# Optimization experiments

Measured on AMD Instinct MI355X. Metric: run time of the kernel, lower is better.

## Reference

```python
import jax, jax.numpy as jnp
import numpy as np

D_MODEL = 384
D_INNER = 768   # 2 * d_model
D_STATE = 16
DT_RANK = 24    # ceil(d_model/16)
K_CONV = 4
BATCH = 8
SEQ = 2048
EPS = 1e-5


def _layer_norm(x, w, b):
    mu = x.mean(-1, keepdims=True)
    var = ((x - mu) ** 2).mean(-1, keepdims=True)
    return (x - mu) * jax.lax.rsqrt(var + EPS) * w + b


def _silu(x):
    return x * jax.nn.sigmoid(x)


def _mamba_mixer(x, in_proj, conv_w, conv_b, x_proj, dt_w, dt_b, A_log, Dp, out_proj):
    # x: (B, L, d_model)
    xz = x @ in_proj.T                      # (B, L, 2*d_inner)
    xs, z = jnp.split(xz, 2, axis=-1)       # each (B, L, d_inner)
    # causal depthwise conv1d (pad left k-1)
    xc = jnp.transpose(xs, (0, 2, 1))       # (B, d_inner, L)
    xc = jnp.pad(xc, ((0, 0), (0, 0), (K_CONV - 1, 0)))
    xc = jax.lax.conv_general_dilated(
        xc, conv_w, window_strides=(1,), padding='VALID',
        feature_group_count=D_INNER,
        dimension_numbers=('NCH', 'OIH', 'NCH'))
    xs = _silu(jnp.transpose(xc, (0, 2, 1)) + conv_b)   # (B, L, d_inner)
    # input-dependent SSM parameters
    x_dbl = xs @ x_proj.T                    # (B, L, dt_rank + 2*d_state)
    dt, Bm, Cm = jnp.split(x_dbl, [DT_RANK, DT_RANK + D_STATE], axis=-1)
    dt = jax.nn.softplus(dt @ dt_w.T + dt_b)  # (B, L, d_inner)
    A = -jnp.exp(A_log)                       # (d_inner, d_state)

    def step(h, inp):
        dt_t, B_t, C_t, x_t = inp             # (B,d), (B,N), (B,N), (B,d)
        h = jnp.exp(dt_t[:, :, None] * A) * h + (dt_t * x_t)[:, :, None] * B_t[:, None, :]
        y = jnp.einsum('bdn,bn->bd', h, C_t)
        return h, y

    h0 = jnp.zeros((xs.shape[0], D_INNER, D_STATE), xs.dtype)
    inps = (jnp.moveaxis(dt, 1, 0), jnp.moveaxis(Bm, 1, 0),
            jnp.moveaxis(Cm, 1, 0), jnp.moveaxis(xs, 1, 0))
    _, ys = jax.lax.scan(step, h0, inps)      # ys: (L, B, d_inner)
    y = jnp.moveaxis(ys, 0, 1) + xs * Dp      # skip term D*x
    y = y * _silu(z)                          # gated output
    return y @ out_proj.T                     # (B, L, d_model)


def setup_inputs() -> dict:
    key = jax.random.key(0)
    ks = jax.random.split(key, 10)
    s = 0.02
    A_init = jnp.broadcast_to(jnp.log(jnp.arange(1, D_STATE + 1, dtype=jnp.float32)),
                              (2, D_INNER, D_STATE))
    return {
        'x': jax.random.normal(ks[0], (BATCH, SEQ, D_MODEL), jnp.float32),
        'norm_w': jnp.ones((2, D_MODEL), jnp.float32),
        'norm_b': jnp.zeros((2, D_MODEL), jnp.float32),
        'in_proj': jax.random.normal(ks[1], (2, 2 * D_INNER, D_MODEL)) * s,
        'conv_w': jax.random.normal(ks[2], (2, D_INNER, 1, K_CONV)) * 0.2,
        'conv_b': jax.random.normal(ks[3], (2, D_INNER)) * s,
        'x_proj': jax.random.normal(ks[4], (2, DT_RANK + 2 * D_STATE, D_INNER)) * s,
        'dt_w': jax.random.normal(ks[5], (2, D_INNER, DT_RANK)) * s,
        'dt_b': jax.random.normal(ks[6], (2, D_INNER)) * 0.1 - 4.0,
        'A_log': A_init,
        'Dp': jnp.ones((2, D_INNER), jnp.float32),
        'out_proj': jax.random.normal(ks[7], (2, D_MODEL, D_INNER)) * s,
    }


def reference(x, norm_w, norm_b, in_proj, conv_w, conv_b, x_proj, dt_w, dt_b, A_log, Dp, out_proj):
    def blk(i, h):
        return h + _mamba_mixer(_layer_norm(h, norm_w[i], norm_b[i]),
                                in_proj[i], conv_w[i], conv_b[i], x_proj[i],
                                dt_w[i], dt_b[i], A_log[i], Dp[i], out_proj[i])
    h = blk(0, x)                    # forward-direction block
    h = jnp.flip(h, axis=-2)         # reverse sequence
    h = blk(1, h)                    # backward-direction block
    return jnp.flip(h, axis=-2)      # restore order
```

## Files before the change

kernel.cpp:

```cpp
#include <hip/hip_runtime.h>
#include <hip/hip_bf16.h>
#include <cstddef>

#define D_MODEL 384
#define D_INNER 768
#define D_STATE 16
#define DT_RANK 24
#define K_CONV  4
#define BATCH   8
#define SEQ     2048
#define BL      (BATCH * SEQ)
#define NCHUNK  128
#define LCHUNK  (SEQ / NCHUNK)
#define XDBL_LD 64
#define LOG2E   1.44269504088896f

typedef unsigned short ushort_t;
typedef __bf16 bf16x8 __attribute__((ext_vector_type(8)));
typedef float  f32x4  __attribute__((ext_vector_type(4)));
typedef unsigned short u16x8 __attribute__((ext_vector_type(8)));

#define GLOBAL_AS(p) ((const __attribute__((address_space(1))) void*)(p))
#define LDS_AS(p)    ((__attribute__((address_space(3))) void*)(p))

__device__ __forceinline__ ushort_t f32_to_bf16_rne(float v) {
    unsigned int u = __float_as_uint(v);
    return (ushort_t)((u + 0x7FFFu + ((u >> 16) & 1u)) >> 16);
}
__device__ __forceinline__ float bf16_to_f32(ushort_t u) {
    return __uint_as_float(((unsigned int)u) << 16);
}

__device__ __forceinline__ void pow_tree16(float w1, float* pw) {
    float w2 = w1 * w1, w4 = w2 * w2, w8 = w4 * w4;
    pw[0] = w1;        pw[1] = w2;        pw[2] = w2 * w1;   pw[3] = w4;
    pw[4] = w4 * w1;   pw[5] = w4 * w2;   pw[6] = w4 * pw[2]; pw[7] = w8;
    pw[8] = w8 * w1;   pw[9] = w8 * w2;   pw[10] = w8 * pw[2]; pw[11] = w8 * w4;
    pw[12] = w8 * pw[4]; pw[13] = w8 * pw[5]; pw[14] = w8 * pw[6]; pw[15] = w8 * w8;
}

__global__ __launch_bounds__(256) void cast_bf16_kernel(
    const float* __restrict__ in, ushort_t* __restrict__ out, int n)
{
    int i = blockIdx.x * 256 + threadIdx.x;
    if (i < n) out[i] = f32_to_bf16_rne(in[i]);
}

__global__ __launch_bounds__(256) void cast_xproj_kernel(
    const float* __restrict__ in, ushort_t* __restrict__ out)
{
    int i = blockIdx.x * 256 + threadIdx.x;
    if (i >= 2 * 64 * D_INNER) return;
    int c   = i % D_INNER;
    int r   = (i / D_INNER) % 64;
    int dir = i / (64 * D_INNER);
    out[i] = (r < 56) ? f32_to_bf16_rne(in[((size_t)dir * 56 + r) * D_INNER + c])
                      : (ushort_t)0;
}

__global__ __launch_bounds__(256) void prep_transpose_kernel(
    const float* __restrict__ conv_w, const float* __restrict__ A_log,
    const float* __restrict__ dt_w, float* __restrict__ cwt,
    float* __restrict__ alt, float* __restrict__ dwt)
{
    int i = blockIdx.x * 256 + threadIdx.x;
    const int NCW = 2 * K_CONV * D_INNER;
    const int NAL = 2 * D_STATE * D_INNER;
    const int NDW = 2 * DT_RANK * D_INNER;
    if (i < NCW) {
        int c = i % D_INNER, k = (i / D_INNER) % K_CONV, dir = i / (K_CONV * D_INNER);
        cwt[i] = conv_w[((size_t)dir * D_INNER + c) * K_CONV + k];
    } else if (i < NCW + NAL) {
        int j = i - NCW;
        int d = j % D_INNER, n = (j / D_INNER) % D_STATE, dir = j / (D_STATE * D_INNER);
        alt[j] = A_log[((size_t)dir * D_INNER + d) * D_STATE + n];
    } else if (i < NCW + NAL + NDW) {
        int j = i - NCW - NAL;
        int d = j % D_INNER, r = (j / D_INNER) % DT_RANK, dir = j / (DT_RANK * D_INNER);
        dwt[j] = dt_w[((size_t)dir * D_INNER + d) * DT_RANK + r];
    }
}

__global__ __launch_bounds__(256) void check_A_kernel(
    const float* __restrict__ A_log, int* __restrict__ flags)
{
    __shared__ int ok[2];
    int tid = threadIdx.x;
    if (tid < 2) ok[tid] = 1;
    __syncthreads();
    for (int dir = 0; dir < 2; dir++) {
        bool good = true;
        for (int j = tid; j < D_INNER * D_STATE; j += 256) {
            int n = j % D_STATE;
            float v = __expf(A_log[(size_t)dir * D_INNER * D_STATE + j]);
            good = good && (fabsf(v - (float)(n + 1)) <= 1e-4f * (float)(n + 1));
        }
        if (!good) atomicAnd(&ok[dir], 0);
    }
    __syncthreads();
    if (tid < 2) flags[tid] = ok[tid];
}

__global__ __launch_bounds__(384) void ln_kernel(
    const float* __restrict__ in, const float* __restrict__ w,
    const float* __restrict__ b, ushort_t* __restrict__ out)
{
    int row = blockIdx.x;
    int tid = threadIdx.x;
    float v = in[(size_t)row * D_MODEL + tid];
    float s = v, sq = v * v;
    #pragma unroll
    for (int o = 32; o; o >>= 1) {
        s  += __shfl_down(s, o);
        sq += __shfl_down(sq, o);
    }
    __shared__ float ss[6], ssq[6];
    __shared__ float mb[2];
    int wid = tid >> 6;
    if ((tid & 63) == 0) { ss[wid] = s; ssq[wid] = sq; }
    __syncthreads();
    if (tid == 0) {
        float S = 0.f, Q = 0.f;
        #pragma unroll
        for (int k = 0; k < 6; k++) { S += ss[k]; Q += ssq[k]; }
        float mu  = S * (1.0f / D_MODEL);
        float var = Q * (1.0f / D_MODEL) - mu * mu;
        mb[0] = mu;
        mb[1] = rsqrtf(var + 1e-5f);
    }
    __syncthreads();
    float r = (v - mb[0]) * mb[1] * w[tid] + b[tid];
    out[(size_t)row * D_MODEL + tid] = f32_to_bf16_rne(r);
}

__global__ __launch_bounds__(256) void gemm_mfma_b16(
    const ushort_t* __restrict__ A, const ushort_t* __restrict__ W,
    ushort_t* __restrict__ C, int N, int K)
{
    __shared__ __bf16 As[128 * 32];
    __shared__ __bf16 Ws[128 * 32];
    int tid  = threadIdx.x;
    int bm = blockIdx.x, bn = blockIdx.y;
    int lane = tid & 63, wave = tid >> 6;
    int wr = wave >> 1, wc = wave & 1;
    int quad = lane >> 4, l16 = lane & 15;

    const ushort_t* Ag = A + (size_t)(bm * 128 + (tid >> 2)) * K + (tid & 3) * 8;
    const ushort_t* Wg = W + (size_t)(bn * 128 + (tid >> 2)) * K + (tid & 3) * 8;

    f32x4 acc[4][4] = {};

    for (int k0 = 0; k0 < K; k0 += 32) {
        __syncthreads();
        __builtin_amdgcn_global_load_lds(GLOBAL_AS(Ag + k0),
                                         LDS_AS(As + tid * 8), 16, 0, 0);
        __builtin_amdgcn_global_load_lds(GLOBAL_AS(Ag + (size_t)64 * K + k0),
                                         LDS_AS(As + 2048 + tid * 8), 16, 0, 0);
        __builtin_amdgcn_global_load_lds(GLOBAL_AS(Wg + k0),
                                         LDS_AS(Ws + tid * 8), 16, 0, 0);
        __builtin_amdgcn_global_load_lds(GLOBAL_AS(Wg + (size_t)64 * K + k0),
                                         LDS_AS(Ws + 2048 + tid * 8), 16, 0, 0);
        __syncthreads();

        bf16x8 af[4], wf[4];
        #pragma unroll
        for (int i = 0; i < 4; i++)
            af[i] = *(const bf16x8*)(As + (wr * 64 + i * 16 + l16) * 32 + quad * 8);
        #pragma unroll
        for (int j = 0; j < 4; j++)
            wf[j] = *(const bf16x8*)(Ws + (wc * 64 + j * 16 + l16) * 32 + quad * 8);
        #pragma unroll
        for (int i = 0; i < 4; i++)
            #pragma unroll
            for (int j = 0; j < 4; j++)
                acc[i][j] = __builtin_amdgcn_mfma_f32_16x16x32_bf16(
                    af[i], wf[j], acc[i][j], 0, 0, 0);
    }

    #pragma unroll
    for (int i = 0; i < 4; i++) {
        #pragma unroll
        for (int r = 0; r < 4; r++) {
            int row = bm * 128 + wr * 64 + i * 16 + quad * 4 + r;
            #pragma unroll
            for (int j = 0; j < 4; j++) {
                int col = bn * 128 + wc * 64 + j * 16 + l16;
                C[(size_t)row * N + col] = f32_to_bf16_rne(acc[i][j][r]);
            }
        }
    }
}

__global__ __launch_bounds__(256) void gemm_mfma_f32(
    const ushort_t* __restrict__ A, const ushort_t* __restrict__ W,
    const float* __restrict__ resid, float* __restrict__ C, int N, int K)
{
    __shared__ __bf16 As[128 * 32];
    __shared__ __bf16 Ws[128 * 32];
    int tid  = threadIdx.x;
    int bm = blockIdx.x, bn = blockIdx.y;
    int lane = tid & 63, wave = tid >> 6;
    int wr = wave >> 1, wc = wave & 1;
    int quad = lane >> 4, l16 = lane & 15;

    const ushort_t* Ag = A + (size_t)(bm * 128 + (tid >> 2)) * K + (tid & 3) * 8;
    const ushort_t* Wg = W + (size_t)(bn * 128 + (tid >> 2)) * K + (tid & 3) * 8;

    f32x4 acc[4][4] = {};

    for (int k0 = 0; k0 < K; k0 += 32) {
        __syncthreads();
        __builtin_amdgcn_global_load_lds(GLOBAL_AS(Ag + k0),
                                         LDS_AS(As + tid * 8), 16, 0, 0);
        __builtin_amdgcn_global_load_lds(GLOBAL_AS(Ag + (size_t)64 * K + k0),
                                         LDS_AS(As + 2048 + tid * 8), 16, 0, 0);
        __builtin_amdgcn_global_load_lds(GLOBAL_AS(Wg + k0),
                                         LDS_AS(Ws + tid * 8), 16, 0, 0);
        __builtin_amdgcn_global_load_lds(GLOBAL_AS(Wg + (size_t)64 * K + k0),
                                         LDS_AS(Ws + 2048 + tid * 8), 16, 0, 0);
        __syncthreads();

        bf16x8 af[4], wf[4];
        #pragma unroll
        for (int i = 0; i < 4; i++)
            af[i] = *(const bf16x8*)(As + (wr * 64 + i * 16 + l16) * 32 + quad * 8);
        #pragma unroll
        for (int j = 0; j < 4; j++)
            wf[j] = *(const bf16x8*)(Ws + (wc * 64 + j * 16 + l16) * 32 + quad * 8);
        #pragma unroll
        for (int i = 0; i < 4; i++)
            #pragma unroll
            for (int j = 0; j < 4; j++)
                acc[i][j] = __builtin_amdgcn_mfma_f32_16x16x32_bf16(
                    af[i], wf[j], acc[i][j], 0, 0, 0);
    }

    #pragma unroll
    for (int i = 0; i < 4; i++) {
        #pragma unroll
        for (int r = 0; r < 4; r++) {
            int row = bm * 128 + wr * 64 + i * 16 + quad * 4 + r;
            #pragma unroll
            for (int j = 0; j < 4; j++) {
                int col = bn * 128 + wc * 64 + j * 16 + l16;
                size_t idx = (size_t)row * N + col;
                C[idx] = acc[i][j][r] + resid[idx];
            }
        }
    }
}

__global__ __launch_bounds__(256) void xdbl_mfma(
    const ushort_t* __restrict__ A, const ushort_t* __restrict__ W,
    float* __restrict__ C)
{
    __shared__ __bf16 As[128 * 32];
    __shared__ __bf16 Ws[64 * 32];
    int tid  = threadIdx.x;
    int bm = blockIdx.x;
    int lane = tid & 63, wave = tid >> 6;
    int quad = lane >> 4, l16 = lane & 15;

    const ushort_t* Ag = A + (size_t)(bm * 128 + (tid >> 2)) * D_INNER + (tid & 3) * 8;
    const ushort_t* Wg = W + (size_t)(tid >> 2) * D_INNER + (tid & 3) * 8;

    f32x4 acc[2][4] = {};

    for (int k0 = 0; k0 < D_INNER; k0 += 32) {
        __syncthreads();
        __builtin_amdgcn_global_load_lds(GLOBAL_AS(Ag + k0),
                                         LDS_AS(As + tid * 8), 16, 0, 0);
        __builtin_amdgcn_global_load_lds(GLOBAL_AS(Ag + (size_t)64 * D_INNER + k0),
                                         LDS_AS(As + 2048 + tid * 8), 16, 0, 0);
        __builtin_amdgcn_global_load_lds(GLOBAL_AS(Wg + k0),
                                         LDS_AS(Ws + tid * 8), 16, 0, 0);
        __syncthreads();

        bf16x8 af[2], wf[4];
        #pragma unroll
        for (int i = 0; i < 2; i++)
            af[i] = *(const bf16x8*)(As + (wave * 32 + i * 16 + l16) * 32 + quad * 8);
        #pragma unroll
        for (int j = 0; j < 4; j++)
            wf[j] = *(const bf16x8*)(Ws + (j * 16 + l16) * 32 + quad * 8);
        #pragma unroll
        for (int i = 0; i < 2; i++)
            #pragma unroll
            for (int j = 0; j < 4; j++)
                acc[i][j] = __builtin_amdgcn_mfma_f32_16x16x32_bf16(
                    af[i], wf[j], acc[i][j], 0, 0, 0);
    }

    #pragma unroll
    for (int i = 0; i < 2; i++) {
        #pragma unroll
        for (int r = 0; r < 4; r++) {
            int row = bm * 128 + wave * 32 + i * 16 + quad * 4 + r;
            #pragma unroll
            for (int j = 0; j < 4; j++) {
                int col = j * 16 + l16;
                C[(size_t)row * XDBL_LD + col] = acc[i][j][r];
            }
        }
    }
}

__global__ __launch_bounds__(256) void dt_kernel(
    const float* __restrict__ xdbl, const float* __restrict__ dwt,
    const float* __restrict__ dtbias, ushort_t* __restrict__ dtb)
{
    int g    = blockIdx.x % 3;
    int row0 = (blockIdx.x / 3) * 16;
    int tid  = threadIdx.x;
    int d    = g * 256 + tid;
    float w[DT_RANK];
    #pragma unroll
    for (int r = 0; r < DT_RANK; r++) w[r] = dwt[r * D_INNER + d];
    float bias = dtbias[d];
    __shared__ float xd[16][DT_RANK];
    if (tid < 16 * DT_RANK) {
        int rr = tid / DT_RANK, cc = tid % DT_RANK;
        xd[rr][cc] = xdbl[(size_t)(row0 + rr) * XDBL_LD + cc];
    }
    __syncthreads();
    #pragma unroll 4
    for (int i = 0; i < 16; i++) {
        float acc = bias;
        #pragma unroll
        for (int r = 0; r < DT_RANK; r++) acc = fmaf(xd[i][r], w[r], acc);
        float sp = acc > 20.f ? acc : __logf(1.f + __expf(acc));
        dtb[(size_t)(row0 + i) * D_INNER + d] = f32_to_bf16_rne(sp);
    }
}

__global__ __launch_bounds__(256) void conv_silu_kernel(
    const ushort_t* __restrict__ xz, const float* __restrict__ cwt,
    const float* __restrict__ cb, ushort_t* __restrict__ xsc, int dir)
{
    int idx8 = blockIdx.x * 256 + threadIdx.x;
    int c8   = (idx8 % 96) * 8;
    int row  = idx8 / 96;
    int l    = row % SEQ;
    int b0   = row - l;

    float acc[8];
    float4 bv0 = *(const float4*)(cb + c8);
    float4 bv1 = *(const float4*)(cb + c8 + 4);
    acc[0] = bv0.x; acc[1] = bv0.y; acc[2] = bv0.z; acc[3] = bv0.w;
    acc[4] = bv1.x; acc[5] = bv1.y; acc[6] = bv1.z; acc[7] = bv1.w;

    #pragma unroll
    for (int k = 0; k < 4; k++) {
        int ls = dir ? (l + k) : (l - 3 + k);
        int wk = dir ? (3 - k) : k;
        bool ok = dir ? (ls < SEQ) : (ls >= 0);
        if (ok) {
            u16x8 v = *(const u16x8*)(xz + (size_t)(b0 + ls) * 1536 + c8);
            float4 w0 = *(const float4*)(cwt + wk * D_INNER + c8);
            float4 w1 = *(const float4*)(cwt + wk * D_INNER + c8 + 4);
            float wv[8] = {w0.x, w0.y, w0.z, w0.w, w1.x, w1.y, w1.z, w1.w};
            #pragma unroll
            for (int j = 0; j < 8; j++)
                acc[j] = fmaf(bf16_to_f32(v[j]), wv[j], acc[j]);
        }
    }
    u16x8 o;
    #pragma unroll
    for (int j = 0; j < 8; j++) {
        float sg = 1.0f / (1.0f + __expf(-acc[j]));
        o[j] = f32_to_bf16_rne(acc[j] * sg);
    }
    *(u16x8*)(xsc + (size_t)row * D_INNER + c8) = o;
}

__global__ __launch_bounds__(256) void scan_pass1(
    const ushort_t* __restrict__ xsc, const ushort_t* __restrict__ dtb,
    const float* __restrict__ xdbl, const float* __restrict__ alt,
    const int* __restrict__ flag,
    ushort_t* __restrict__ hstate, float* __restrict__ sumdt_buf, int dir)
{
    int g = blockIdx.x % 3;
    int c = (blockIdx.x / 3) % NCHUNK;
    int b = blockIdx.x / (3 * NCHUNK);
    int d = g * 256 + threadIdx.x;
    float h[D_STATE] = {};
    float sdt = 0.f;
    size_t base = (size_t)b * SEQ;

    if (flag[0]) {
        for (int i = 0; i < LCHUNK; i++) {
            int p = c * LCHUNK + i;
            int l = dir ? (SEQ - 1 - p) : p;
            size_t row = base + l;
            float dtv = bf16_to_f32(dtb[row * D_INNER + d]);
            float xv  = bf16_to_f32(xsc[row * D_INNER + d]);
            float dtx = dtv * xv;
            sdt += dtv;
            const float* Br = xdbl + row * XDBL_LD + DT_RANK;
            float pw[D_STATE];
            pow_tree16(__builtin_amdgcn_exp2f(-dtv * LOG2E), pw);
            #pragma unroll
            for (int n = 0; n < D_STATE; n++)
                h[n] = fmaf(pw[n], h[n], dtx * Br[n]);
        }
    } else {
        float A2[D_STATE];
        #pragma unroll
        for (int n = 0; n < D_STATE; n++)
            A2[n] = -__expf(alt[n * D_INNER + d]) * LOG2E;
        for (int i = 0; i < LCHUNK; i++) {
            int p = c * LCHUNK + i;
            int l = dir ? (SEQ - 1 - p) : p;
            size_t row = base + l;
            float dtv = bf16_to_f32(dtb[row * D_INNER + d]);
            float xv  = bf16_to_f32(xsc[row * D_INNER + d]);
            float dtx = dtv * xv;
            sdt += dtv;
            const float* Br = xdbl + row * XDBL_LD + DT_RANK;
            #pragma unroll
            for (int n = 0; n < D_STATE; n++)
                h[n] = fmaf(__builtin_amdgcn_exp2f(dtv * A2[n]), h[n], dtx * Br[n]);
        }
    }
    size_t cidx = (size_t)(b * NCHUNK + c) * D_INNER + d;
    sumdt_buf[cidx] = sdt;
    #pragma unroll
    for (int n = 0; n < D_STATE; n++)
        hstate[cidx * D_STATE + n] = f32_to_bf16_rne(h[n]);
}

__global__ __launch_bounds__(256) void scan_pass2(
    ushort_t* __restrict__ hstate, const float* __restrict__ sumdt_buf,
    const float* __restrict__ alt)
{
    int gid = blockIdx.x * 256 + threadIdx.x;
    int n = gid & 15;
    int d = (gid >> 4) % D_INNER;
    int b = gid / (16 * D_INNER);
    float A2 = -__expf(alt[n * D_INNER + d]) * LOG2E;
    float h = 0.f;
    for (int c = 0; c < NCHUNK; c++) {
        size_t cidx = (size_t)(b * NCHUNK + c) * D_INNER + d;
        float ho = bf16_to_f32(hstate[cidx * D_STATE + n]);
        hstate[cidx * D_STATE + n] = f32_to_bf16_rne(h);
        h = fmaf(__builtin_amdgcn_exp2f(A2 * sumdt_buf[cidx]), h, ho);
    }
}

__global__ __launch_bounds__(256) void scan_pass3(
    const ushort_t* __restrict__ xsc, const ushort_t* __restrict__ dtb,
    const ushort_t* __restrict__ xz, const float* __restrict__ xdbl,
    const float* __restrict__ alt, const float* __restrict__ Dp,
    const int* __restrict__ flag, const ushort_t* __restrict__ hstate,
    ushort_t* __restrict__ y, int dir)
{
    int g = blockIdx.x % 3;
    int c = (blockIdx.x / 3) % NCHUNK;
    int b = blockIdx.x / (3 * NCHUNK);
    int d = g * 256 + threadIdx.x;
    size_t cidx = (size_t)(b * NCHUNK + c) * D_INNER + d;
    float h[D_STATE];
    #pragma unroll
    for (int n = 0; n < D_STATE; n++)
        h[n] = bf16_to_f32(hstate[cidx * D_STATE + n]);
    float Dd = Dp[d];
    size_t base = (size_t)b * SEQ;

    if (flag[0]) {
        for (int i = 0; i < LCHUNK; i++) {
            int p = c * LCHUNK + i;
            int l = dir ? (SEQ - 1 - p) : p;
            size_t row = base + l;
            float dtv = bf16_to_f32(dtb[row * D_INNER + d]);
            float xv  = bf16_to_f32(xsc[row * D_INNER + d]);
            float zv  = bf16_to_f32(xz[row * 1536 + D_INNER + d]);
            float dtx = dtv * xv;
            const float* Br = xdbl + row * XDBL_LD + DT_RANK;
            const float* Cr = Br + D_STATE;
            float pw[D_STATE];
            pow_tree16(__builtin_amdgcn_exp2f(-dtv * LOG2E), pw);
            float yv = 0.f;
            #pragma unroll
            for (int n = 0; n < D_STATE; n++) {
                h[n] = fmaf(pw[n], h[n], dtx * Br[n]);
                yv = fmaf(h[n], Cr[n], yv);
            }
            yv = fmaf(xv, Dd, yv);
            float sg = 1.f / (1.f + __expf(-zv));
            yv *= zv * sg;
            y[row * D_INNER + d] = f32_to_bf16_rne(yv);
        }
    } else {
        float A2[D_STATE];
        #pragma unroll
        for (int n = 0; n < D_STATE; n++)
            A2[n] = -__expf(alt[n * D_INNER + d]) * LOG2E;
        for (int i = 0; i < LCHUNK; i++) {
            int p = c * LCHUNK + i;
            int l = dir ? (SEQ - 1 - p) : p;
            size_t row = base + l;
            float dtv = bf16_to_f32(dtb[row * D_INNER + d]);
            float xv  = bf16_to_f32(xsc[row * D_INNER + d]);
            float zv  = bf16_to_f32(xz[row * 1536 + D_INNER + d]);
            float dtx = dtv * xv;
            const float* Br = xdbl + row * XDBL_LD + DT_RANK;
            const float* Cr = Br + D_STATE;
            float yv = 0.f;
            #pragma unroll
            for (int n = 0; n < D_STATE; n++) {
                h[n] = fmaf(__builtin_amdgcn_exp2f(dtv * A2[n]), h[n], dtx * Br[n]);
                yv = fmaf(h[n], Cr[n], yv);
            }
            yv = fmaf(xv, Dd, yv);
            float sg = 1.f / (1.f + __expf(-zv));
            yv *= zv * sg;
            y[row * D_INNER + d] = f32_to_bf16_rne(yv);
        }
    }
}

extern "C" void kernel_launch(void* const* d_in, const int* in_sizes, int n_in,
                              void* d_out, int out_size, void* d_ws, size_t ws_size,
                              hipStream_t stream)
{
    const float* x       = (const float*)d_in[0];
    const float* norm_w  = (const float*)d_in[1];
    const float* norm_b  = (const float*)d_in[2];
    const float* in_proj = (const float*)d_in[3];
    const float* conv_w  = (const float*)d_in[4];
    const float* conv_b  = (const float*)d_in[5];
    const float* x_proj  = (const float*)d_in[6];
    const float* dt_w    = (const float*)d_in[7];
    const float* dt_b    = (const float*)d_in[8];
    const float* A_log   = (const float*)d_in[9];
    const float* Dp      = (const float*)d_in[10];
    const float* out_proj= (const float*)d_in[11];
    float* out = (float*)d_out;

    float* ws   = (float*)d_ws;
    float* reg0 = ws;                ws += (size_t)BL * D_INNER / 2;
    ushort_t* lnb = (ushort_t*)reg0;
    ushort_t* ybf = (ushort_t*)reg0;
    ushort_t* xzb  = (ushort_t*)ws;  ws += (size_t)BL * 1536 / 2;
    ushort_t* xscb = (ushort_t*)ws;  ws += (size_t)BL * D_INNER / 2;
    ushort_t* dtb  = (ushort_t*)ws;  ws += (size_t)BL * D_INNER / 2;
    float* xdbl = ws;                ws += (size_t)BL * XDBL_LD;
    float* sumdt  = ws;              ws += (size_t)BATCH * NCHUNK * D_INNER;
    ushort_t* hstate = (ushort_t*)ws; ws += (size_t)BATCH * NCHUNK * D_INNER * D_STATE / 2;
    ushort_t* wbf_in  = (ushort_t*)ws;  ws += (size_t)2 * 1536 * D_MODEL / 2;
    ushort_t* wbf_out = (ushort_t*)ws;  ws += (size_t)2 * D_MODEL * D_INNER / 2;
    ushort_t* xp_bf   = (ushort_t*)ws;  ws += (size_t)2 * 64 * D_INNER / 2;
    float* cwt = ws;                 ws += (size_t)2 * K_CONV * D_INNER;
    float* alt = ws;                 ws += (size_t)2 * D_STATE * D_INNER;
    float* dwt = ws;                 ws += (size_t)2 * DT_RANK * D_INNER;
    int* aflags = (int*)ws;          ws += 2;

    cast_bf16_kernel<<<(2 * 1536 * D_MODEL + 255) / 256, 256, 0, stream>>>(
        in_proj, wbf_in, 2 * 1536 * D_MODEL);
    cast_bf16_kernel<<<(2 * D_MODEL * D_INNER + 255) / 256, 256, 0, stream>>>(
        out_proj, wbf_out, 2 * D_MODEL * D_INNER);
    cast_xproj_kernel<<<(2 * 64 * D_INNER + 255) / 256, 256, 0, stream>>>(
        x_proj, xp_bf);
    {
        int total = 2 * (K_CONV + D_STATE + DT_RANK) * D_INNER;
        prep_transpose_kernel<<<(total + 255) / 256, 256, 0, stream>>>(
            conv_w, A_log, dt_w, cwt, alt, dwt);
    }
    check_A_kernel<<<1, 256, 0, stream>>>(A_log, aflags);

    for (int i = 0; i < 2; i++) {
        const float* hinp = (i == 0) ? x : out;
        ln_kernel<<<BL, 384, 0, stream>>>(hinp, norm_w + i * D_MODEL,
                                          norm_b + i * D_MODEL, lnb);
        gemm_mfma_b16<<<dim3(BL / 128, 1536 / 128), 256, 0, stream>>>(
            lnb, wbf_in + (size_t)i * 1536 * D_MODEL, xzb, 1536, D_MODEL);
        conv_silu_kernel<<<(BL * 96) / 256, 256, 0, stream>>>(
            xzb, cwt + (size_t)i * K_CONV * D_INNER, conv_b + i * D_INNER,
            xscb, i);
        xdbl_mfma<<<BL / 128, 256, 0, stream>>>(
            xscb, xp_bf + (size_t)i * 64 * D_INNER, xdbl);
        dt_kernel<<<(BL / 16) * 3, 256, 0, stream>>>(
            xdbl, dwt + (size_t)i * DT_RANK * D_INNER, dt_b + i * D_INNER, dtb);
        scan_pass1<<<BATCH * NCHUNK * 3, 256, 0, stream>>>(
            xscb, dtb, xdbl, alt + (size_t)i * D_STATE * D_INNER,
            aflags + i, hstate, sumdt, i);
        scan_pass2<<<(BATCH * D_INNER * D_STATE) / 256, 256, 0, stream>>>(
            hstate, sumdt, alt + (size_t)i * D_STATE * D_INNER);
        scan_pass3<<<BATCH * NCHUNK * 3, 256, 0, stream>>>(
            xscb, dtb, xzb, xdbl, alt + (size_t)i * D_STATE * D_INNER,
            Dp + i * D_INNER, aflags + i, hstate, ybf, i);
        gemm_mfma_f32<<<dim3(BL / 128, D_MODEL / 128), 256, 0, stream>>>(
            ybf, wbf_out + (size_t)i * D_MODEL * D_INNER, hinp, out,
            D_MODEL, D_INNER);
    }
}
```

Measured before the change: 499.8 us.

## Halve scan chunk count, widen GEMM K-tile to 64, merge prep kernels

Three separate changes. The chunked scan now uses 64 chunks instead of 128, so each chunk is longer and fewer chunk states are stored and combined. Both MFMA GEMMs now stage a 64-wide K slab per iteration instead of 32, which halves the barrier count and doubles LDS use. The four weight cast and transpose kernels are merged into one launch to cut launch overhead. The trade-offs are less scan parallelism per pass and lower occupancy from the larger LDS footprint.

```diff
diff --git a/kernel.cpp b/kernel.cpp
--- a/kernel.cpp
+++ b/kernel.cpp
@@ -10,7 +10,7 @@
 #define BATCH   8
 #define SEQ     2048
 #define BL      (BATCH * SEQ)
-#define NCHUNK  128
+#define NCHUNK  64
 #define LCHUNK  (SEQ / NCHUNK)
 #define XDBL_LD 64
 #define LOG2E   1.44269504088896f
@@ -39,45 +39,58 @@
     pw[12] = w8 * pw[4]; pw[13] = w8 * pw[5]; pw[14] = w8 * pw[6]; pw[15] = w8 * w8;
 }
 
-__global__ __launch_bounds__(256) void cast_bf16_kernel(
-    const float* __restrict__ in, ushort_t* __restrict__ out, int n)
+#define N_INP  (2 * 1536 * D_MODEL)
+#define N_OUTP (2 * D_MODEL * D_INNER)
+#define N_XP   (2 * 64 * D_INNER)
+#define N_CW   (2 * K_CONV * D_INNER)
+#define N_AL   (2 * D_STATE * D_INNER)
+#define N_DW   (2 * DT_RANK * D_INNER)
+#define N_PREP (N_INP + N_OUTP + N_XP + N_CW + N_AL + N_DW)
+
+__global__ __launch_bounds__(256) void prep_kernel(
+    const float* __restrict__ in_proj, const float* __restrict__ out_proj,
+    const float* __restrict__ x_proj, const float* __restrict__ conv_w,
+    const float* __restrict__ A_log, const float* __restrict__ dt_w,
+    ushort_t* __restrict__ wbf_in, ushort_t* __restrict__ wbf_out,
+    ushort_t* __restrict__ xp_bf, float* __restrict__ cwt,
+    float* __restrict__ alt, float* __restrict__ dwt)
 {
     int i = blockIdx.x * 256 + threadIdx.x;
-    if (i < n) out[i] = f32_to_bf16_rne(in[i]);
-}
-
-__global__ __launch_bounds__(256) void cast_xproj_kernel(
-    const float* __restrict__ in, ushort_t* __restrict__ out)
-{
-    int i = blockIdx.x * 256 + threadIdx.x;
-    if (i >= 2 * 64 * D_INNER) return;
-    int c   = i % D_INNER;
-    int r   = (i / D_INNER) % 64;
-    int dir = i / (64 * D_INNER);
-    out[i] = (r < 56) ? f32_to_bf16_rne(in[((size_t)dir * 56 + r) * D_INNER + c])
-                      : (ushort_t)0;
-}
-
-__global__ __launch_bounds__(256) void prep_transpose_kernel(
-    const float* __restrict__ conv_w, const float* __restrict__ A_log,
-    const float* __restrict__ dt_w, float* __restrict__ cwt,
-    float* __restrict__ alt, float* __restrict__ dwt)
-{
-    int i = blockIdx.x * 256 + threadIdx.x;
-    const int NCW = 2 * K_CONV * D_INNER;
-    const int NAL = 2 * D_STATE * D_INNER;
-    const int NDW = 2 * DT_RANK * D_INNER;
-    if (i < NCW) {
+    if (i < N_INP) {
+        wbf_in[i] = f32_to_bf16_rne(in_proj[i]);
+        return;
+    }
+    i -= N_INP;
+    if (i < N_OUTP) {
+        wbf_out[i] = f32_to_bf16_rne(out_proj[i]);
+        return;
+    }
+    i -= N_OUTP;
+    if (i < N_XP) {
+        int c   = i % D_INNER;
+        int r   = (i / D_INNER) % 64;
+        int dir = i / (64 * D_INNER);
+        xp_bf[i] = (r < 56)
+            ? f32_to_bf16_rne(x_proj[((size_t)dir * 56 + r) * D_INNER + c])
+            : (ushort_t)0;
+        return;
+    }
+    i -= N_XP;
+    if (i < N_CW) {
         int c = i % D_INNER, k = (i / D_INNER) % K_CONV, dir = i / (K_CONV * D_INNER);
         cwt[i] = conv_w[((size_t)dir * D_INNER + c) * K_CONV + k];
-    } else if (i < NCW + NAL) {
-        int j = i - NCW;
-        int d = j % D_INNER, n = (j / D_INNER) % D_STATE, dir = j / (D_STATE * D_INNER);
-        alt[j] = A_log[((size_t)dir * D_INNER + d) * D_STATE + n];
-    } else if (i < NCW + NAL + NDW) {
-        int j = i - NCW - NAL;
-        int d = j % D_INNER, r = (j / D_INNER) % DT_RANK, dir = j / (DT_RANK * D_INNER);
-        dwt[j] = dt_w[((size_t)dir * D_INNER + d) * DT_RANK + r];
+        return;
+    }
+    i -= N_CW;
+    if (i < N_AL) {
+        int d = i % D_INNER, n = (i / D_INNER) % D_STATE, dir = i / (D_STATE * D_INNER);
+        alt[i] = A_log[((size_t)dir * D_INNER + d) * D_STATE + n];
+        return;
+    }
+    i -= N_AL;
+    if (i < N_DW) {
+        int d = i % D_INNER, r = (i / D_INNER) % DT_RANK, dir = i / (DT_RANK * D_INNER);
+        dwt[i] = dt_w[((size_t)dir * D_INNER + d) * DT_RANK + r];
     }
 }
 
@@ -137,44 +150,48 @@
     const ushort_t* __restrict__ A, const ushort_t* __restrict__ W,
     ushort_t* __restrict__ C, int N, int K)
 {
-    __shared__ __bf16 As[128 * 32];
-    __shared__ __bf16 Ws[128 * 32];
+    __shared__ __bf16 As[128 * 64];
+    __shared__ __bf16 Ws[128 * 64];
     int tid  = threadIdx.x;
     int bm = blockIdx.x, bn = blockIdx.y;
     int lane = tid & 63, wave = tid >> 6;
     int wr = wave >> 1, wc = wave & 1;
     int quad = lane >> 4, l16 = lane & 15;
 
-    const ushort_t* Ag = A + (size_t)(bm * 128 + (tid >> 2)) * K + (tid & 3) * 8;
-    const ushort_t* Wg = W + (size_t)(bn * 128 + (tid >> 2)) * K + (tid & 3) * 8;
+    const ushort_t* Ag = A + (size_t)(bm * 128 + (tid >> 3)) * K + (tid & 7) * 8;
+    const ushort_t* Wg = W + (size_t)(bn * 128 + (tid >> 3)) * K + (tid & 7) * 8;
 
     f32x4 acc[4][4] = {};
 
-    for (int k0 = 0; k0 < K; k0 += 32) {
+    for (int k0 = 0; k0 < K; k0 += 64) {
         __syncthreads();
-        __builtin_amdgcn_global_load_lds(GLOBAL_AS(Ag + k0),
-                                         LDS_AS(As + tid * 8), 16, 0, 0);
-        __builtin_amdgcn_global_load_lds(GLOBAL_AS(Ag + (size_t)64 * K + k0),
-                                         LDS_AS(As + 2048 + tid * 8), 16, 0, 0);
-        __builtin_amdgcn_global_load_lds(GLOBAL_AS(Wg + k0),
-                                         LDS_AS(Ws + tid * 8), 16, 0, 0);
-        __builtin_amdgcn_global_load_lds(GLOBAL_AS(Wg + (size_t)64 * K + k0),
-                                         LDS_AS(Ws + 2048 + tid * 8), 16, 0, 0);
+        #pragma unroll
+        for (int s = 0; s < 4; s++) {
+            __builtin_amdgcn_global_load_lds(
+                GLOBAL_AS(Ag + (size_t)(s * 32) * K + k0),
+                LDS_AS(As + s * 2048 + tid * 8), 16, 0, 0);
+            __builtin_amdgcn_global_load_lds(
+                GLOBAL_AS(Wg + (size_t)(s * 32) * K + k0),
+                LDS_AS(Ws + s * 2048 + tid * 8), 16, 0, 0);
+        }
         __syncthreads();
 
-        bf16x8 af[4], wf[4];
-        #pragma unroll
-        for (int i = 0; i < 4; i++)
-            af[i] = *(const bf16x8*)(As + (wr * 64 + i * 16 + l16) * 32 + quad * 8);
-        #pragma unroll
-        for (int j = 0; j < 4; j++)
-            wf[j] = *(const bf16x8*)(Ws + (wc * 64 + j * 16 + l16) * 32 + quad * 8);
-        #pragma unroll
-        for (int i = 0; i < 4; i++)
+        #pragma unroll
+        for (int ks = 0; ks < 64; ks += 32) {
+            bf16x8 af[4], wf[4];
+            #pragma unroll
+            for (int i = 0; i < 4; i++)
+                af[i] = *(const bf16x8*)(As + (wr * 64 + i * 16 + l16) * 64 + ks + quad * 8);
             #pragma unroll
             for (int j = 0; j < 4; j++)
-                acc[i][j] = __builtin_amdgcn_mfma_f32_16x16x32_bf16(
-                    af[i], wf[j], acc[i][j], 0, 0, 0);
+                wf[j] = *(const bf16x8*)(Ws + (wc * 64 + j * 16 + l16) * 64 + ks + quad * 8);
+            #pragma unroll
+            for (int i = 0; i < 4; i++)
+                #pragma unroll
+                for (int j = 0; j < 4; j++)
+                    acc[i][j] = __builtin_amdgcn_mfma_f32_16x16x32_bf16(
+                        af[i], wf[j], acc[i][j], 0, 0, 0);
+        }
     }
 
     #pragma unroll
@@ -195,44 +212,48 @@
     const ushort_t* __restrict__ A, const ushort_t* __restrict__ W,
     const float* __restrict__ resid, float* __restrict__ C, int N, int K)
 {
-    __shared__ __bf16 As[128 * 32];
-    __shared__ __bf16 Ws[128 * 32];
+    __shared__ __bf16 As[128 * 64];
+    __shared__ __bf16 Ws[128 * 64];
     int tid  = threadIdx.x;
     int bm = blockIdx.x, bn = blockIdx.y;
     int lane = tid & 63, wave = tid >> 6;
     int wr = wave >> 1, wc = wave & 1;
     int quad = lane >> 4, l16 = lane & 15;
 
-    const ushort_t* Ag = A + (size_t)(bm * 128 + (tid >> 2)) * K + (tid & 3) * 8;
-    const ushort_t* Wg = W + (size_t)(bn * 128 + (tid >> 2)) * K + (tid & 3) * 8;
+    const ushort_t* Ag = A + (size_t)(bm * 128 + (tid >> 3)) * K + (tid & 7) * 8;
+    const ushort_t* Wg = W + (size_t)(bn * 128 + (tid >> 3)) * K + (tid & 7) * 8;
 
     f32x4 acc[4][4] = {};
 
-    for (int k0 = 0; k0 < K; k0 += 32) {
+    for (int k0 = 0; k0 < K; k0 += 64) {
         __syncthreads();
-        __builtin_amdgcn_global_load_lds(GLOBAL_AS(Ag + k0),
-                                         LDS_AS(As + tid * 8), 16, 0, 0);
-        __builtin_amdgcn_global_load_lds(GLOBAL_AS(Ag + (size_t)64 * K + k0),
-                                         LDS_AS(As + 2048 + tid * 8), 16, 0, 0);
-        __builtin_amdgcn_global_load_lds(GLOBAL_AS(Wg + k0),
-                                         LDS_AS(Ws + tid * 8), 16, 0, 0);
-        __builtin_amdgcn_global_load_lds(GLOBAL_AS(Wg + (size_t)64 * K + k0),
-                                         LDS_AS(Ws + 2048 + tid * 8), 16, 0, 0);
+        #pragma unroll
+        for (int s = 0; s < 4; s++) {
+            __builtin_amdgcn_global_load_lds(
+                GLOBAL_AS(Ag + (size_t)(s * 32) * K + k0),
+                LDS_AS(As + s * 2048 + tid * 8), 16, 0, 0);
+            __builtin_amdgcn_global_load_lds(
+                GLOBAL_AS(Wg + (size_t)(s * 32) * K + k0),
+                LDS_AS(Ws + s * 2048 + tid * 8), 16, 0, 0);
+        }
         __syncthreads();
 
-        bf16x8 af[4], wf[4];
-        #pragma unroll
-        for (int i = 0; i < 4; i++)
-            af[i] = *(const bf16x8*)(As + (wr * 64 + i * 16 + l16) * 32 + quad * 8);
-        #pragma unroll
-        for (int j = 0; j < 4; j++)
-            wf[j] = *(const bf16x8*)(Ws + (wc * 64 + j * 16 + l16) * 32 + quad * 8);
-        #pragma unroll
-        for (int i = 0; i < 4; i++)
+        #pragma unroll
+        for (int ks = 0; ks < 64; ks += 32) {
+            bf16x8 af[4], wf[4];
+            #pragma unroll
+            for (int i = 0; i < 4; i++)
+                af[i] = *(const bf16x8*)(As + (wr * 64 + i * 16 + l16) * 64 + ks + quad * 8);
             #pragma unroll
             for (int j = 0; j < 4; j++)
-                acc[i][j] = __builtin_amdgcn_mfma_f32_16x16x32_bf16(
-                    af[i], wf[j], acc[i][j], 0, 0, 0);
+                wf[j] = *(const bf16x8*)(Ws + (wc * 64 + j * 16 + l16) * 64 + ks + quad * 8);
+            #pragma unroll
+            for (int i = 0; i < 4; i++)
+                #pragma unroll
+                for (int j = 0; j < 4; j++)
+                    acc[i][j] = __builtin_amdgcn_mfma_f32_16x16x32_bf16(
+                        af[i], wf[j], acc[i][j], 0, 0, 0);
+        }
     }
 
     #pragma unroll
@@ -547,25 +568,17 @@
     float* xdbl = ws;                ws += (size_t)BL * XDBL_LD;
     float* sumdt  = ws;              ws += (size_t)BATCH * NCHUNK * D_INNER;
     ushort_t* hstate = (ushort_t*)ws; ws += (size_t)BATCH * NCHUNK * D_INNER * D_STATE / 2;
-    ushort_t* wbf_in  = (ushort_t*)ws;  ws += (size_t)2 * 1536 * D_MODEL / 2;
-    ushort_t* wbf_out = (ushort_t*)ws;  ws += (size_t)2 * D_MODEL * D_INNER / 2;
-    ushort_t* xp_bf   = (ushort_t*)ws;  ws += (size_t)2 * 64 * D_INNER / 2;
-    float* cwt = ws;                 ws += (size_t)2 * K_CONV * D_INNER;
-    float* alt = ws;                 ws += (size_t)2 * D_STATE * D_INNER;
-    float* dwt = ws;                 ws += (size_t)2 * DT_RANK * D_INNER;
+    ushort_t* wbf_in  = (ushort_t*)ws;  ws += (size_t)N_INP / 2;
+    ushort_t* wbf_out = (ushort_t*)ws;  ws += (size_t)N_OUTP / 2;
+    ushort_t* xp_bf   = (ushort_t*)ws;  ws += (size_t)N_XP / 2;
+    float* cwt = ws;                 ws += (size_t)N_CW;
+    float* alt = ws;                 ws += (size_t)N_AL;
+    float* dwt = ws;                 ws += (size_t)N_DW;
     int* aflags = (int*)ws;          ws += 2;
 
-    cast_bf16_kernel<<<(2 * 1536 * D_MODEL + 255) / 256, 256, 0, stream>>>(
-        in_proj, wbf_in, 2 * 1536 * D_MODEL);
-    cast_bf16_kernel<<<(2 * D_MODEL * D_INNER + 255) / 256, 256, 0, stream>>>(
-        out_proj, wbf_out, 2 * D_MODEL * D_INNER);
-    cast_xproj_kernel<<<(2 * 64 * D_INNER + 255) / 256, 256, 0, stream>>>(
-        x_proj, xp_bf);
-    {
-        int total = 2 * (K_CONV + D_STATE + DT_RANK) * D_INNER;
-        prep_transpose_kernel<<<(total + 255) / 256, 256, 0, stream>>>(
-            conv_w, A_log, dt_w, cwt, alt, dwt);
-    }
+    prep_kernel<<<N_PREP / 256, 256, 0, stream>>>(
+        in_proj, out_proj, x_proj, conv_w, A_log, dt_w,
+        wbf_in, wbf_out, xp_bf, cwt, alt, dwt);
     check_A_kernel<<<1, 256, 0, stream>>>(A_log, aflags);
 
     for (int i = 0; i < 2; i++) {
```

Measured after the change: 494.1 us. Within noise of the previous version (-1.1%).
